# Performance work log

Hardware: AMD Instinct MI355X
Metric: run time of the kernel (lower is better)

## Reference

```python
import jax, jax.numpy as jnp
import numpy as np

N_E, N_IN = 1024, 64
HIDDEN, OUT = 128, 64


def setup_inputs() -> dict:
    key = jax.random.key(0)
    kx, k1, k2 = jax.random.split(key, 3)
    x = jax.random.normal(kx, (N_E, N_IN), dtype=jnp.float32)
    # edge-MLP params: Dense(2*n_in -> HIDDEN) + tanh + Dense(HIDDEN -> OUT)
    W1 = jax.random.normal(k1, (2 * N_IN, HIDDEN), dtype=jnp.float32) / np.sqrt(2 * N_IN)
    b1 = jnp.zeros((HIDDEN,), dtype=jnp.float32)
    W2 = jax.random.normal(k2, (HIDDEN, OUT), dtype=jnp.float32) / np.sqrt(HIDDEN)
    b2 = jnp.zeros((OUT,), dtype=jnp.float32)
    return {"x": x, "W1": W1, "b1": b1, "W2": W2, "b2": b2}


def reference(x, W1, b1, W2, b2):
    n_e, n_in = x.shape
    # modular all-pairs index: partner of i is (i + j) % n_e for j in 1..n_e-1
    pair_idx = (jnp.arange(n_e)[:, None] + jnp.arange(1, n_e)[None, :]) % n_e  # [n_e, n_e-1]
    # pairs[i, j] = concat(x[i], x[pair_idx[i, j]])  -> [n_e, n_e-1, 2*n_in]
    self_feat = jnp.broadcast_to(x[:, None, :], (n_e, n_e - 1, n_in))
    pairs = jnp.concatenate([self_feat, x[pair_idx]], axis=-1)
    # edge MLP: Dense + tanh + Dense
    h = jnp.tanh(jnp.einsum("epf,fh->eph", pairs, W1) + b1)
    upd = jnp.einsum("eph,ho->epo", h, W2) + b2
    # mean over partners
    return jnp.mean(upd, axis=1)  # [n_e, OUT]
```

## Files before the change

### kernel.cpp

```cpp
#include <hip/hip_runtime.h>
#include <math.h>


#define N_E  1024
#define NIN  64
#define HID  128
#define OUTD 64
#define PCH  30
#define NQ   64
#define S_CH 5.5f

static constexpr float INV_S     = 1.0f / 5.5f;
static constexpr float TWO_LOG2E = 2.8853900817779268f;

__global__ __launch_bounds__(256) void prep_coeff_kernel(
    const float* __restrict__ x, const float* __restrict__ W1,
    const float* __restrict__ b1,
    float* __restrict__ A, float* __restrict__ B,
    float* __restrict__ C, float* __restrict__ M) {
  const int t = threadIdx.x;
  if (blockIdx.x < N_E / 2) {
    __shared__ float xs[2][NIN];
    const int sub = t >> 7, h = t & (HID - 1);
    const int i = blockIdx.x * 2 + sub;
    if (t < 2 * NIN) xs[t >> 6][t & 63] = x[(blockIdx.x * 2 + (t >> 6)) * NIN + (t & 63)];
    __syncthreads();
    float accA = 0.f, accB = 0.f;
    #pragma unroll 8
    for (int f = 0; f < NIN; ++f) {
      const float xv = xs[sub][f];
      accA += xv * W1[f * HID + h];
      accB += xv * W1[(NIN + f) * HID + h];
    }
    A[i * HID + h] = accA;
    B[i * HID + h] = accB + b1[h];
  } else {
    __shared__ double ctab[2 * NQ];
    __shared__ double fg[(NQ + 1) * (NQ + 1)];
    __shared__ double G[PCH * (NQ + 1)];
    for (int m = t; m < 2 * NQ; m += 256) ctab[m] = cos((double)m * (M_PI / NQ));
    for (int idx = t; idx < PCH * HID; idx += 256) M[idx] = 0.f;
    __syncthreads();
    for (int idx = t; idx < (NQ + 1) * (NQ + 1); idx += 256) {
      const int j = idx / (NQ + 1), l = idx % (NQ + 1);
      fg[idx] = tanh((double)S_CH * (ctab[j] + ctab[l]));
    }
    __syncthreads();
    for (int idx = t; idx < PCH * (NQ + 1); idx += 256) {
      const int q = idx / (NQ + 1), j = idx % (NQ + 1);
      double s = 0.0;
      for (int l = 0; l <= NQ; ++l) {
        const double w = (l == 0 || l == NQ) ? 0.5 : 1.0;
        s += w * fg[j * (NQ + 1) + l] * ctab[(q * l) & (2 * NQ - 1)];
      }
      G[idx] = s;
    }
    __syncthreads();
    for (int idx = t; idx < PCH * PCH; idx += 256) {
      const int p = idx / PCH, q = idx % PCH;
      double s = 0.0;
      for (int j = 0; j <= NQ; ++j) {
        const double w = (j == 0 || j == NQ) ? 0.5 : 1.0;
        s += w * G[q * (NQ + 1) + j] * ctab[(p * j) & (2 * NQ - 1)];
      }
      const double cp = (p == 0 ? 1.0 : 2.0) / NQ;
      const double cq = (q == 0 ? 1.0 : 2.0) / NQ;
      C[idx] = (float)(s * cp * cq);
    }
  }
}

__global__ __launch_bounds__(256) void moments_kernel(
    const float* __restrict__ B, float* __restrict__ M) {
  __shared__ float Msub[PCH][256];
  const int t = threadIdx.x;
  const int h = t & (HID - 1), sub = t >> 7;
  float acc[PCH];
  #pragma unroll
  for (int q = 0; q < PCH; ++q) acc[q] = 0.f;
  const int k0 = blockIdx.x * 16 + sub * 8;
  for (int j = 0; j < 8; ++j) {
    float b = B[(k0 + j) * HID + h];
    b = fminf(fmaxf(b, -S_CH), S_CH) * INV_S;
    float t0 = 1.f, t1 = b;
    const float b2x = b + b;
    acc[0] += 1.f;
    acc[1] += b;
    #pragma unroll
    for (int q = 2; q < PCH; ++q) {
      const float t2 = b2x * t1 - t0;
      acc[q] += t2;
      t0 = t1; t1 = t2;
    }
  }
  #pragma unroll
  for (int q = 0; q < PCH; ++q) Msub[q][t] = acc[q];
  __syncthreads();
  for (int idx = t; idx < PCH * HID; idx += 256) {
    const int q = idx / HID, hh = idx % HID;
    atomicAdd(&M[q * HID + hh], Msub[q][hh] + Msub[q][hh + HID]);
  }
}

__global__ __launch_bounds__(HID) void v_kernel(
    const float* __restrict__ C, const float* __restrict__ M,
    float* __restrict__ V) {
  const int p = blockIdx.x, h = threadIdx.x;
  float acc = 0.f;
  #pragma unroll
  for (int q = 0; q < PCH; ++q) acc += C[p * PCH + q] * M[q * HID + h];
  V[p * HID + h] = acc;
}

__global__ __launch_bounds__(HID) void combine_out_kernel(
    const float* __restrict__ A, const float* __restrict__ B,
    const float* __restrict__ V, const float* __restrict__ W2,
    const float* __restrict__ b2, float* __restrict__ out) {
  __shared__ float Sl[HID];
  __shared__ float red[2][OUTD];
  const int i = blockIdx.x, h = threadIdx.x;
  const float ar = A[i * HID + h], br = B[i * HID + h];
  const float a = fminf(fmaxf(ar, -S_CH), S_CH) * INV_S;
  float t0 = 1.f, t1 = a;
  const float a2x = a + a;
  float acc = V[h] + a * V[HID + h];
  #pragma unroll
  for (int p = 2; p < PCH; ++p) {
    const float t2 = a2x * t1 - t0;
    acc += t2 * V[p * HID + h];
    t0 = t1; t1 = t2;
  }
  const float vs = ar + br;
  const float ts = 1.f - 2.f * __builtin_amdgcn_rcpf(1.f + __builtin_amdgcn_exp2f(vs * TWO_LOG2E));
  Sl[h] = (acc - ts) * (1.f / (float)(N_E - 1));
  __syncthreads();
  const int o = h & (OUTD - 1), half = h >> 6;
  const int h0 = half * 64;
  float po = 0.f;
  #pragma unroll 16
  for (int hh = 0; hh < 64; ++hh)
    po += Sl[h0 + hh] * W2[(h0 + hh) * OUTD + o];
  red[half][o] = po;
  __syncthreads();
  if (h < OUTD) out[i * OUTD + h] = red[0][h] + red[1][h] + b2[h];
}

extern "C" void kernel_launch(void* const* d_in, const int* in_sizes, int n_in,
                              void* d_out, int out_size, void* d_ws, size_t ws_size,
                              hipStream_t stream) {
  const float* x  = (const float*)d_in[0];
  const float* W1 = (const float*)d_in[1];
  const float* b1 = (const float*)d_in[2];
  const float* W2 = (const float*)d_in[3];
  const float* b2 = (const float*)d_in[4];
  float* out = (float*)d_out;

  float* A = (float*)d_ws;
  float* B = A + N_E * HID;
  float* M = B + N_E * HID;
  float* V = M + PCH * HID;
  float* C = V + PCH * HID;

  prep_coeff_kernel<<<N_E / 2 + 1, 256, 0, stream>>>(x, W1, b1, A, B, C, M);
  moments_kernel<<<N_E / 16, 256, 0, stream>>>(B, M);
  v_kernel<<<PCH, HID, 0, stream>>>(C, M, V);
  combine_out_kernel<<<N_E, HID, 0, stream>>>(A, B, V, W2, b2, out);
}
```

Measured before the change: 95.29 us.

## Fuse four kernels into two, compute coefficients in float, drop atomics

Collapses the four-launch pipeline into two kernels. The first builds the Chebyshev coefficient matrix in float with a smaller quadrature (NQ 32 instead of 64) and writes per-partition B moments without atomics. The second reduces the partitions, forms V, recomputes A and B from x and W1, and does the W2 projection four rows per block. This removes launch overhead, the A/B workspace round trip and double-precision work. The trade-offs are lower coefficient accuracy and a serial moment pass over only 16 blocks.

```diff
diff --git a/kernel.cpp b/kernel.cpp
--- a/kernel.cpp
+++ b/kernel.cpp
@@ -1,148 +1,192 @@
 #include <hip/hip_runtime.h>
-#include <math.h>
-
-
-#define N_E  1024
-#define NIN  64
-#define HID  128
-#define OUTD 64
-#define PCH  30
-#define NQ   64
-#define S_CH 5.5f
+
+
+#define N_E   1024
+#define NIN   64
+#define HID   128
+#define OUTD  64
+#define PCH   30
+#define NQ    32
+#define NPART 16
+#define S_CH  5.5f
 
 static constexpr float INV_S     = 1.0f / 5.5f;
 static constexpr float TWO_LOG2E = 2.8853900817779268f;
-
-__global__ __launch_bounds__(256) void prep_coeff_kernel(
+static constexpr float PI_F      = 3.14159265358979323846f;
+
+__device__ __forceinline__ float tanh_fast(float u) {
+  return 1.0f - 2.0f * __builtin_amdgcn_rcpf(
+      1.0f + __builtin_amdgcn_exp2f(u * TWO_LOG2E));
+}
+
+__global__ __launch_bounds__(256, 1) void k1_coeff_moments(
     const float* __restrict__ x, const float* __restrict__ W1,
     const float* __restrict__ b1,
-    float* __restrict__ A, float* __restrict__ B,
-    float* __restrict__ C, float* __restrict__ M) {
+    float* __restrict__ C, float* __restrict__ Mpart) {
   const int t = threadIdx.x;
-  if (blockIdx.x < N_E / 2) {
-    __shared__ float xs[2][NIN];
-    const int sub = t >> 7, h = t & (HID - 1);
-    const int i = blockIdx.x * 2 + sub;
-    if (t < 2 * NIN) xs[t >> 6][t & 63] = x[(blockIdx.x * 2 + (t >> 6)) * NIN + (t & 63)];
-    __syncthreads();
-    float accA = 0.f, accB = 0.f;
-    #pragma unroll 8
-    for (int f = 0; f < NIN; ++f) {
-      const float xv = xs[sub][f];
-      accA += xv * W1[f * HID + h];
-      accB += xv * W1[(NIN + f) * HID + h];
-    }
-    A[i * HID + h] = accA;
-    B[i * HID + h] = accB + b1[h];
-  } else {
-    __shared__ double ctab[2 * NQ];
-    __shared__ double fg[(NQ + 1) * (NQ + 1)];
-    __shared__ double G[PCH * (NQ + 1)];
-    for (int m = t; m < 2 * NQ; m += 256) ctab[m] = cos((double)m * (M_PI / NQ));
-    for (int idx = t; idx < PCH * HID; idx += 256) M[idx] = 0.f;
+  if (blockIdx.x == 0) {
+    __shared__ float ctab[NQ + 1];
+    __shared__ float fg[(NQ + 1) * (NQ + 2)];
+    __shared__ float G[PCH * (NQ + 2)];
+    if (t <= NQ) ctab[t] = cosf((float)t * (PI_F / (float)NQ));
     __syncthreads();
     for (int idx = t; idx < (NQ + 1) * (NQ + 1); idx += 256) {
       const int j = idx / (NQ + 1), l = idx % (NQ + 1);
-      fg[idx] = tanh((double)S_CH * (ctab[j] + ctab[l]));
+      fg[j * (NQ + 2) + l] = tanh_fast(S_CH * (ctab[j] + ctab[l]));
     }
     __syncthreads();
     for (int idx = t; idx < PCH * (NQ + 1); idx += 256) {
       const int q = idx / (NQ + 1), j = idx % (NQ + 1);
-      double s = 0.0;
-      for (int l = 0; l <= NQ; ++l) {
-        const double w = (l == 0 || l == NQ) ? 0.5 : 1.0;
-        s += w * fg[j * (NQ + 1) + l] * ctab[(q * l) & (2 * NQ - 1)];
+      const float cphi = ctab[q];
+      float c0 = 1.f, c1 = cphi;
+      float s = 0.5f * fg[j * (NQ + 2) + 0];
+      for (int l = 1; l <= NQ; ++l) {
+        const float w = (l == NQ) ? 0.5f : 1.0f;
+        s += w * fg[j * (NQ + 2) + l] * c1;
+        const float c2 = 2.f * cphi * c1 - c0; c0 = c1; c1 = c2;
       }
-      G[idx] = s;
+      G[q * (NQ + 2) + j] = s;
     }
     __syncthreads();
     for (int idx = t; idx < PCH * PCH; idx += 256) {
       const int p = idx / PCH, q = idx % PCH;
-      double s = 0.0;
-      for (int j = 0; j <= NQ; ++j) {
-        const double w = (j == 0 || j == NQ) ? 0.5 : 1.0;
-        s += w * G[q * (NQ + 1) + j] * ctab[(p * j) & (2 * NQ - 1)];
+      const float cphi = ctab[p];
+      float c0 = 1.f, c1 = cphi;
+      float s = 0.5f * G[q * (NQ + 2) + 0];
+      for (int j = 1; j <= NQ; ++j) {
+        const float w = (j == NQ) ? 0.5f : 1.0f;
+        s += w * G[q * (NQ + 2) + j] * c1;
+        const float c2 = 2.f * cphi * c1 - c0; c0 = c1; c1 = c2;
       }
-      const double cp = (p == 0 ? 1.0 : 2.0) / NQ;
-      const double cq = (q == 0 ? 1.0 : 2.0) / NQ;
-      C[idx] = (float)(s * cp * cq);
-    }
-  }
-}
-
-__global__ __launch_bounds__(256) void moments_kernel(
-    const float* __restrict__ B, float* __restrict__ M) {
-  __shared__ float Msub[PCH][256];
+      const float cp = (p == 0 ? 1.f : 2.f) / (float)NQ;
+      const float cq = (q == 0 ? 1.f : 2.f) / (float)NQ;
+      C[p * PCH + q] = s * cp * cq;
+    }
+  } else {
+    const int part = blockIdx.x - 1;
+    const int h = t & (HID - 1), half = t >> 7;
+    float w1c[NIN];
+    #pragma unroll
+    for (int f = 0; f < NIN; ++f) w1c[f] = W1[(NIN + f) * HID + h];
+    const float b1h = b1[h];
+    float acc[PCH];
+    #pragma unroll
+    for (int q = 0; q < PCH; ++q) acc[q] = 0.f;
+    const int k0 = part * 64 + half * 32;
+    for (int kk = 0; kk < 32; ++kk) {
+      const float* __restrict__ xr = x + (k0 + kk) * NIN;
+      float b = b1h;
+      #pragma unroll
+      for (int f = 0; f < NIN; ++f) b += xr[f] * w1c[f];
+      const float u = fminf(fmaxf(b, -S_CH), S_CH) * INV_S;
+      acc[0] += 1.f;
+      acc[1] += u;
+      float t0 = 1.f, t1 = u;
+      const float u2 = u + u;
+      #pragma unroll
+      for (int q = 2; q < PCH; ++q) {
+        const float t2 = u2 * t1 - t0;
+        acc[q] += t2;
+        t0 = t1; t1 = t2;
+      }
+    }
+    __shared__ float Msub[PCH][256];
+    #pragma unroll
+    for (int q = 0; q < PCH; ++q) Msub[q][t] = acc[q];
+    __syncthreads();
+    float* __restrict__ Mp = Mpart + part * PCH * HID;
+    for (int idx = t; idx < PCH * HID; idx += 256) {
+      const int q = idx >> 7, hh = idx & (HID - 1);
+      Mp[idx] = Msub[q][hh] + Msub[q][hh + HID];
+    }
+  }
+}
+
+__global__ __launch_bounds__(256, 1) void k2_combine_out(
+    const float* __restrict__ x, const float* __restrict__ W1,
+    const float* __restrict__ b1, const float* __restrict__ W2,
+    const float* __restrict__ b2, const float* __restrict__ C,
+    const float* __restrict__ Mpart, float* __restrict__ out) {
   const int t = threadIdx.x;
   const int h = t & (HID - 1), sub = t >> 7;
-  float acc[PCH];
-  #pragma unroll
-  for (int q = 0; q < PCH; ++q) acc[q] = 0.f;
-  const int k0 = blockIdx.x * 16 + sub * 8;
-  for (int j = 0; j < 8; ++j) {
-    float b = B[(k0 + j) * HID + h];
-    b = fminf(fmaxf(b, -S_CH), S_CH) * INV_S;
-    float t0 = 1.f, t1 = b;
-    const float b2x = b + b;
-    acc[0] += 1.f;
-    acc[1] += b;
-    #pragma unroll
-    for (int q = 2; q < PCH; ++q) {
-      const float t2 = b2x * t1 - t0;
-      acc[q] += t2;
+  __shared__ float Vs[2][PCH][HID];
+  __shared__ float Sl[4][HID];
+
+  float m[PCH / 2];
+  #pragma unroll
+  for (int qq = 0; qq < PCH / 2; ++qq) {
+    const int q = sub * (PCH / 2) + qq;
+    float s = 0.f;
+    #pragma unroll
+    for (int part = 0; part < NPART; ++part)
+      s += Mpart[part * PCH * HID + q * HID + h];
+    m[qq] = s;
+  }
+  #pragma unroll
+  for (int p = 0; p < PCH; ++p) {
+    float s = 0.f;
+    #pragma unroll
+    for (int qq = 0; qq < PCH / 2; ++qq)
+      s += C[p * PCH + sub * (PCH / 2) + qq] * m[qq];
+    Vs[sub][p][h] = s;
+  }
+  __syncthreads();
+  float v[PCH];
+  #pragma unroll
+  for (int p = 0; p < PCH; ++p) v[p] = Vs[0][p][h] + Vs[1][p][h];
+
+  const int i0 = blockIdx.x * 4 + sub * 2;
+  const float* __restrict__ x0 = x + i0 * NIN;
+  const float* __restrict__ x1 = x + (i0 + 1) * NIN;
+  float w1c[NIN];
+  #pragma unroll
+  for (int f = 0; f < NIN; ++f) w1c[f] = W1[f * HID + h];
+  float a0 = 0.f, a1 = 0.f;
+  #pragma unroll
+  for (int f = 0; f < NIN; ++f) {
+    a0 += x0[f] * w1c[f];
+    a1 += x1[f] * w1c[f];
+  }
+  #pragma unroll
+  for (int f = 0; f < NIN; ++f) w1c[f] = W1[(NIN + f) * HID + h];
+  const float b1h = b1[h];
+  float bb0 = b1h, bb1 = b1h;
+  #pragma unroll
+  for (int f = 0; f < NIN; ++f) {
+    bb0 += x0[f] * w1c[f];
+    bb1 += x1[f] * w1c[f];
+  }
+  #pragma unroll
+  for (int r = 0; r < 2; ++r) {
+    const float ar = r ? a1 : a0;
+    const float br = r ? bb1 : bb0;
+    const float ua = fminf(fmaxf(ar, -S_CH), S_CH) * INV_S;
+    float s = v[0] + ua * v[1];
+    float t0 = 1.f, t1 = ua;
+    const float ua2 = ua + ua;
+    #pragma unroll
+    for (int p = 2; p < PCH; ++p) {
+      const float t2 = ua2 * t1 - t0;
+      s += t2 * v[p];
       t0 = t1; t1 = t2;
     }
-  }
-  #pragma unroll
-  for (int q = 0; q < PCH; ++q) Msub[q][t] = acc[q];
+    const float self = tanh_fast(ar + br);
+    Sl[sub * 2 + r][h] = (s - self) * (1.0f / (float)(N_E - 1));
+  }
   __syncthreads();
-  for (int idx = t; idx < PCH * HID; idx += 256) {
-    const int q = idx / HID, hh = idx % HID;
-    atomicAdd(&M[q * HID + hh], Msub[q][hh] + Msub[q][hh + HID]);
-  }
-}
-
-__global__ __launch_bounds__(HID) void v_kernel(
-    const float* __restrict__ C, const float* __restrict__ M,
-    float* __restrict__ V) {
-  const int p = blockIdx.x, h = threadIdx.x;
-  float acc = 0.f;
-  #pragma unroll
-  for (int q = 0; q < PCH; ++q) acc += C[p * PCH + q] * M[q * HID + h];
-  V[p * HID + h] = acc;
-}
-
-__global__ __launch_bounds__(HID) void combine_out_kernel(
-    const float* __restrict__ A, const float* __restrict__ B,
-    const float* __restrict__ V, const float* __restrict__ W2,
-    const float* __restrict__ b2, float* __restrict__ out) {
-  __shared__ float Sl[HID];
-  __shared__ float red[2][OUTD];
-  const int i = blockIdx.x, h = threadIdx.x;
-  const float ar = A[i * HID + h], br = B[i * HID + h];
-  const float a = fminf(fmaxf(ar, -S_CH), S_CH) * INV_S;
-  float t0 = 1.f, t1 = a;
-  const float a2x = a + a;
-  float acc = V[h] + a * V[HID + h];
-  #pragma unroll
-  for (int p = 2; p < PCH; ++p) {
-    const float t2 = a2x * t1 - t0;
-    acc += t2 * V[p * HID + h];
-    t0 = t1; t1 = t2;
-  }
-  const float vs = ar + br;
-  const float ts = 1.f - 2.f * __builtin_amdgcn_rcpf(1.f + __builtin_amdgcn_exp2f(vs * TWO_LOG2E));
-  Sl[h] = (acc - ts) * (1.f / (float)(N_E - 1));
-  __syncthreads();
-  const int o = h & (OUTD - 1), half = h >> 6;
-  const int h0 = half * 64;
-  float po = 0.f;
-  #pragma unroll 16
-  for (int hh = 0; hh < 64; ++hh)
-    po += Sl[h0 + hh] * W2[(h0 + hh) * OUTD + o];
-  red[half][o] = po;
-  __syncthreads();
-  if (h < OUTD) out[i * OUTD + h] = red[0][h] + red[1][h] + b2[h];
+  const int o = t & (OUTD - 1), r4 = t >> 6;
+  const float4* __restrict__ slr = (const float4*)&Sl[r4][0];
+  float accO = b2[o];
+  #pragma unroll
+  for (int hh4 = 0; hh4 < HID / 4; ++hh4) {
+    const float4 sv = slr[hh4];
+    const int hb = hh4 * 4;
+    accO += sv.x * W2[(hb + 0) * OUTD + o];
+    accO += sv.y * W2[(hb + 1) * OUTD + o];
+    accO += sv.z * W2[(hb + 2) * OUTD + o];
+    accO += sv.w * W2[(hb + 3) * OUTD + o];
+  }
+  out[(blockIdx.x * 4 + r4) * OUTD + o] = accO;
 }
 
 extern "C" void kernel_launch(void* const* d_in, const int* in_sizes, int n_in,
@@ -155,14 +199,9 @@
   const float* b2 = (const float*)d_in[4];
   float* out = (float*)d_out;
 
-  float* A = (float*)d_ws;
-  float* B = A + N_E * HID;
-  float* M = B + N_E * HID;
-  float* V = M + PCH * HID;
-  float* C = V + PCH * HID;
-
-  prep_coeff_kernel<<<N_E / 2 + 1, 256, 0, stream>>>(x, W1, b1, A, B, C, M);
-  moments_kernel<<<N_E / 16, 256, 0, stream>>>(B, M);
-  v_kernel<<<PCH, HID, 0, stream>>>(C, M, V);
-  combine_out_kernel<<<N_E, HID, 0, stream>>>(A, B, V, W2, b2, out);
-}
+  float* C     = (float*)d_ws;
+  float* Mpart = C + PCH * PCH;
+
+  k1_coeff_moments<<<1 + NPART, 256, 0, stream>>>(x, W1, b1, C, Mpart);
+  k2_combine_out<<<N_E / 4, 256, 0, stream>>>(x, W1, b1, W2, b2, C, Mpart, out);
+}
```

Result: slower. 106.1 us (+11.3%).
